# Kernel optimization log

Measured on AMD Instinct MI355X. Metric: run time of the kernel, lower is better.

## Reference

```python
import jax, jax.numpy as jnp
import numpy as np
from jax import lax

D = 96          # voxel grid side
N = 131072      # active voxels
C = 128         # channels
EPS = 1e-4
SLOPE_INNER = 0.05      # nn.LeakyReLU(0.05)
SLOPE_OUT = 1.0 / 3.0   # scn.LeakyReLU() default leakiness


def _build_nbr():
    rng = np.random.default_rng(0)
    lin = rng.choice(D ** 3, size=N, replace=False)
    coords = np.stack(np.unravel_index(lin, (D, D, D)), axis=1)  # [N,3]
    lut = -np.ones(D ** 3, dtype=np.int64)
    lut[lin] = np.arange(N)
    nbr = np.full((N, 27), -1, dtype=np.int64)
    k = 0
    for dx in (-1, 0, 1):
        for dy in (-1, 0, 1):
            for dz in (-1, 0, 1):
                nc = coords + np.array([dx, dy, dz])
                valid = ((nc >= 0) & (nc < D)).all(axis=1)
                li = nc[valid, 0] * D * D + nc[valid, 1] * D + nc[valid, 2]
                nbr[valid, k] = lut[li]
                k += 1
    return nbr


def setup_inputs() -> dict:
    key = jax.random.key(0)
    ks = jax.random.split(key, 4)
    ws = 1.0 / np.sqrt(27 * C)
    return {
        "features": jax.random.normal(ks[0], (N, C), jnp.float32),
        "nbr_idx": jnp.asarray(_build_nbr()),
        "w1": jax.random.normal(ks[1], (27, C, C), jnp.float32) * ws,
        "w2": jax.random.normal(ks[2], (27, C, C), jnp.float32) * ws,
        "w3": jax.random.normal(ks[3], (27, C, C), jnp.float32) * ws,
        "g1": jnp.ones((C,), jnp.float32), "b1": jnp.zeros((C,), jnp.float32),
        "g2": jnp.ones((C,), jnp.float32), "b2": jnp.zeros((C,), jnp.float32),
        "g3": jnp.ones((C,), jnp.float32), "b3": jnp.zeros((C,), jnp.float32),
    }


def _subm_conv(feat, nbr, W):
    # feat [N,Cin], nbr [N,27] (-1 = no active neighbor), W [27,Cin,Cout]
    mask = nbr >= 0
    safe = jnp.where(mask, nbr, 0)
    acc0 = jnp.zeros((feat.shape[0], W.shape[-1]), feat.dtype)

    def step(acc, inp):
        idx, m, Wk = inp  # idx [N], m [N], Wk [Cin,Cout]
        g = feat[idx] * m[:, None].astype(feat.dtype)  # gather + mask
        return acc + g @ Wk, None

    out, _ = lax.scan(step, acc0, (safe.T, mask.T, W))
    return out


def _bn(x, g, b):
    # BatchNorm1d with batch stats (track_running_stats=False), biased var
    mu = x.mean(axis=0)
    var = x.var(axis=0)
    return (x - mu) * lax.rsqrt(var + EPS) * g + b


def _lrelu(x, slope):
    return jnp.where(x >= 0, x, slope * x)


def reference(features, nbr_idx, w1, w2, w3, g1, b1, g2, b2, g3, b3):
    x = _lrelu(_bn(_subm_conv(features, nbr_idx, w1), g1, b1), SLOPE_INNER)
    res = x
    x = _lrelu(_bn(_subm_conv(x, nbr_idx, w2), g2, b2), SLOPE_INNER)
    x = _bn(_subm_conv(x, nbr_idx, w3), g3, b3)
    return _lrelu(x + res, SLOPE_OUT)
```

## Files before the change

### kernel.cpp

```cpp
#include <hip/hip_runtime.h>
#include <hip/hip_bf16.h>
#include <stdint.h>

#define NVOX 131072
#define CCH  128
#define EPSV 1e-4f

typedef __bf16 bf16_t;
typedef bf16_t bf16x8 __attribute__((ext_vector_type(8)));
typedef bf16_t bf16x4 __attribute__((ext_vector_type(4)));
typedef float  f32x4  __attribute__((ext_vector_type(4)));

__device__ __forceinline__ void async16(void* lds, const void* g) {
    __builtin_amdgcn_global_load_lds(
        (const __attribute__((address_space(1))) uint32_t*)g,
        (__attribute__((address_space(3))) uint32_t*)lds, 16, 0, 0);
}

__global__ void k_prep_feat(const float* __restrict__ f, bf16_t* __restrict__ fb) {
    int i = blockIdx.x * 256 + threadIdx.x;
    const float4* f4 = (const float4*)f;
    float4 v = f4[i];
    bf16x4 o;
    o[0] = (bf16_t)v.x; o[1] = (bf16_t)v.y; o[2] = (bf16_t)v.z; o[3] = (bf16_t)v.w;
    ((bf16x4*)fb)[i] = o;
}

__global__ void k_prep_misc(bf16_t* featb, bf16_t* xb1, bf16_t* xb2, float* stats) {
    int t = threadIdx.x;
    if (t < 128) {
        featb[(size_t)NVOX * CCH + t] = (bf16_t)0.0f;
        xb1[(size_t)NVOX * CCH + t]   = (bf16_t)0.0f;
        xb2[(size_t)NVOX * CCH + t]   = (bf16_t)0.0f;
    }
    for (int i = t; i < 768; i += 256) stats[i] = 0.0f;
}

__global__ void k_prep_w(const float* __restrict__ w0, const float* __restrict__ w1,
                         const float* __restrict__ w2, bf16_t* __restrict__ wbt) {
    int blk = blockIdx.x;
    int layer = blk / 27, k = blk % 27;
    const float* w = (layer == 0 ? w0 : (layer == 1 ? w1 : w2)) + k * 16384;
    __shared__ bf16_t tile[128][132];
    for (int e = threadIdx.x; e < 16384; e += 256) {
        int ci = e >> 7, co = e & 127;
        tile[co][ci] = (bf16_t)w[e];
    }
    __syncthreads();
    bf16_t* out = wbt + (size_t)blk * 16384;
    for (int e = threadIdx.x; e < 16384; e += 256) {
        int co = e >> 7, ci = e & 127;
        out[e] = tile[co][ci];
    }
}

__global__ __launch_bounds__(256, 3) void k_conv(
        const bf16_t* __restrict__ featb,
        const bf16_t* __restrict__ wbt,
        const int* __restrict__ nbr,
        float* __restrict__ out,
        float* __restrict__ stat)
{
    __shared__ uint32_t offs[27 * 128];
    __shared__ bf16_t smA[128 * 32];
    __shared__ bf16_t smB[128 * 32];
    __shared__ float ssum[128], ssq[128];

    const int tid = threadIdx.x;
    const int m0 = blockIdx.x << 7;

    if (tid < 128) { ssum[tid] = 0.0f; ssq[tid] = 0.0f; }

    for (int e = tid; e < 27 * 128; e += 256) {
        int row = e / 27, k = e - row * 27;
        int idx = nbr[(size_t)(m0 + row) * 27 + k];
        offs[(k << 7) + row] = ((uint32_t)(idx < 0 ? NVOX : idx)) << 8;
    }
    __syncthreads();

    const int l = tid & 63, w = tid >> 6;
    const int wm = w >> 1, wn = w & 1;
    const int lrow = l & 15, lq = l >> 4;

    const int srow = (w << 4) + (l >> 2);
    const int ssub = (l & 3) << 4;

    char* dstA0 = (char*)smA + (w << 10);
    char* dstA1 = (char*)smA + 4096 + (w << 10);
    char* dstB0 = (char*)smB + (w << 10);
    char* dstB1 = (char*)smB + 4096 + (w << 10);

    const char* fbase = (const char*)featb;
    const char* wbase = (const char*)wbt;

    f32x4 acc[4][4] = {};

    for (int k = 0; k < 27; ++k) {
        uint32_t offA0 = offs[(k << 7) + srow];
        uint32_t offA1 = offs[(k << 7) + srow + 64];
        const char* wk = wbase + ((size_t)k << 15);
        #pragma unroll
        for (int c = 0; c < 4; ++c) {
            const int cb = c << 6;
            __syncthreads();
            async16(dstA0, fbase + offA0 + cb + ssub);
            async16(dstA1, fbase + offA1 + cb + ssub);
            async16(dstB0, wk + (srow << 8) + cb + ssub);
            async16(dstB1, wk + ((srow + 64) << 8) + cb + ssub);
            __syncthreads();

            bf16x8 af[4], bfr[4];
            #pragma unroll
            for (int i = 0; i < 4; ++i) {
                af[i]  = *(const bf16x8*)((const char*)smA +
                          ((((wm << 6) + (i << 4) + lrow)) << 6) + (lq << 4));
                bfr[i] = *(const bf16x8*)((const char*)smB +
                          ((((wn << 6) + (i << 4) + lrow)) << 6) + (lq << 4));
            }
            #pragma unroll
            for (int i = 0; i < 4; ++i)
                #pragma unroll
                for (int j = 0; j < 4; ++j)
                    acc[i][j] = __builtin_amdgcn_mfma_f32_16x16x32_bf16(
                        af[i], bfr[j], acc[i][j], 0, 0, 0);
        }
    }

    float csum[4] = {0, 0, 0, 0}, csq[4] = {0, 0, 0, 0};
    #pragma unroll
    for (int j = 0; j < 4; ++j) {
        int col = (wn << 6) + (j << 4) + lrow;
        #pragma unroll
        for (int i = 0; i < 4; ++i) {
            int grow = m0 + (wm << 6) + (i << 4) + (lq << 2);
            #pragma unroll
            for (int r = 0; r < 4; ++r) {
                float v = acc[i][j][r];
                out[(size_t)(grow + r) * CCH + col] = v;
                csum[j] += v;
                csq[j]  += v * v;
            }
        }
    }
    #pragma unroll
    for (int j = 0; j < 4; ++j) {
        csum[j] += __shfl_xor(csum[j], 16, 64);
        csum[j] += __shfl_xor(csum[j], 32, 64);
        csq[j]  += __shfl_xor(csq[j], 16, 64);
        csq[j]  += __shfl_xor(csq[j], 32, 64);
    }
    if (lq == 0) {
        #pragma unroll
        for (int j = 0; j < 4; ++j) {
            int col = (wn << 6) + (j << 4) + lrow;
            atomicAdd(&ssum[col], csum[j]);
            atomicAdd(&ssq[col],  csq[j]);
        }
    }
    __syncthreads();
    if (tid < 128) {
        atomicAdd(&stat[tid],       ssum[tid]);
        atomicAdd(&stat[128 + tid], ssq[tid]);
    }
}

__global__ void k_bnact(const float* __restrict__ x, const float* __restrict__ stat,
                        const float* __restrict__ g, const float* __restrict__ b,
                        bf16_t* __restrict__ out, float slope) {
    __shared__ float sc[128], sh[128];
    int tid = threadIdx.x;
    if (tid < 128) {
        float mu  = stat[tid] * (1.0f / NVOX);
        float var = stat[128 + tid] * (1.0f / NVOX) - mu * mu;
        float inv = rsqrtf(var + EPSV);
        float s = g[tid] * inv;
        sc[tid] = s;
        sh[tid] = b[tid] - mu * s;
    }
    __syncthreads();
    int i = blockIdx.x * 256 + tid;
    float4 v = ((const float4*)x)[i];
    int c = (i << 2) & 127;
    float y0 = v.x * sc[c]     + sh[c];
    float y1 = v.y * sc[c + 1] + sh[c + 1];
    float y2 = v.z * sc[c + 2] + sh[c + 2];
    float y3 = v.w * sc[c + 3] + sh[c + 3];
    y0 = y0 >= 0.0f ? y0 : slope * y0;
    y1 = y1 >= 0.0f ? y1 : slope * y1;
    y2 = y2 >= 0.0f ? y2 : slope * y2;
    y3 = y3 >= 0.0f ? y3 : slope * y3;
    bf16x4 o;
    o[0] = (bf16_t)y0; o[1] = (bf16_t)y1; o[2] = (bf16_t)y2; o[3] = (bf16_t)y3;
    ((bf16x4*)out)[i] = o;
}

__global__ void k_final(const float* __restrict__ x, const float* __restrict__ stat,
                        const float* __restrict__ g, const float* __restrict__ b,
                        const bf16_t* __restrict__ res, float* __restrict__ out) {
    __shared__ float sc[128], sh[128];
    int tid = threadIdx.x;
    if (tid < 128) {
        float mu  = stat[tid] * (1.0f / NVOX);
        float var = stat[128 + tid] * (1.0f / NVOX) - mu * mu;
        float inv = rsqrtf(var + EPSV);
        float s = g[tid] * inv;
        sc[tid] = s;
        sh[tid] = b[tid] - mu * s;
    }
    __syncthreads();
    int i = blockIdx.x * 256 + tid;
    float4 v = ((const float4*)x)[i];
    bf16x4 r = ((const bf16x4*)res)[i];
    int c = (i << 2) & 127;
    float y0 = v.x * sc[c]     + sh[c]     + (float)r[0];
    float y1 = v.y * sc[c + 1] + sh[c + 1] + (float)r[1];
    float y2 = v.z * sc[c + 2] + sh[c + 2] + (float)r[2];
    float y3 = v.w * sc[c + 3] + sh[c + 3] + (float)r[3];
    const float k3 = 1.0f / 3.0f;
    y0 = y0 >= 0.0f ? y0 : k3 * y0;
    y1 = y1 >= 0.0f ? y1 : k3 * y1;
    y2 = y2 >= 0.0f ? y2 : k3 * y2;
    y3 = y3 >= 0.0f ? y3 : k3 * y3;
    float4 o; o.x = y0; o.y = y1; o.z = y2; o.w = y3;
    ((float4*)out)[i] = o;
}

extern "C" void kernel_launch(void* const* d_in, const int* in_sizes, int n_in,
                              void* d_out, int out_size, void* d_ws, size_t ws_size,
                              hipStream_t stream) {
    (void)in_sizes; (void)n_in; (void)out_size; (void)ws_size;
    const float* features = (const float*)d_in[0];
    const int*   nbr      = (const int*)d_in[1];
    const float* w1 = (const float*)d_in[2];
    const float* w2 = (const float*)d_in[3];
    const float* w3 = (const float*)d_in[4];
    const float* g1 = (const float*)d_in[5];
    const float* b1 = (const float*)d_in[6];
    const float* g2 = (const float*)d_in[7];
    const float* b2 = (const float*)d_in[8];
    const float* g3 = (const float*)d_in[9];
    const float* b3 = (const float*)d_in[10];

    char* ws = (char*)d_ws;
    const size_t SZ_FB = (size_t)(NVOX + 1) * CCH * 2;
    bf16_t* featb    = (bf16_t*)(ws);
    bf16_t* xb1      = (bf16_t*)(ws + SZ_FB);
    bf16_t* xb2      = (bf16_t*)(ws + 2 * SZ_FB);
    float*  conv_out = (float*)(ws + 3 * SZ_FB);
    bf16_t* wbt      = (bf16_t*)(ws + 3 * SZ_FB + (size_t)NVOX * CCH * 4);
    float*  stats    = (float*)(ws + 3 * SZ_FB + (size_t)NVOX * CCH * 4
                                + (size_t)3 * 27 * 128 * 128 * 2);

    k_prep_feat<<<16384, 256, 0, stream>>>(features, featb);
    k_prep_misc<<<1, 256, 0, stream>>>(featb, xb1, xb2, stats);
    k_prep_w<<<81, 256, 0, stream>>>(w1, w2, w3, wbt);

    k_conv<<<1024, 256, 0, stream>>>(featb, wbt, nbr, conv_out, stats);
    k_bnact<<<16384, 256, 0, stream>>>(conv_out, stats, g1, b1, xb1, 0.05f);

    k_conv<<<1024, 256, 0, stream>>>(xb1, wbt + (size_t)27 * 16384, nbr, conv_out, stats + 256);
    k_bnact<<<16384, 256, 0, stream>>>(conv_out, stats + 256, g2, b2, xb2, 0.05f);

    k_conv<<<1024, 256, 0, stream>>>(xb2, wbt + (size_t)2 * 27 * 16384, nbr, conv_out, stats + 512);
    k_final<<<16384, 256, 0, stream>>>(conv_out, stats + 512, g3, b3, xb1, (float*)d_out);
}
```

Measured before the change: 538.7 us.

## Triple-buffer conv LDS staging with async prefetch and XOR-swizzled layout

Replaces the single-buffer load/sync/compute loop in the sparse conv GEMM with a flattened 108-step pipeline that keeps two stages of gather and weight loads in flight across three LDS buffers. Only one barrier per step remains, gated by explicit vmcnt waits. It also XOR-swizzles the LDS layout to reduce bank conflicts on fragment reads and raises wave priority around the MFMA block. The extra LDS use forces launch bounds down from 3 to 2 blocks per CU, which lowers occupancy.

```diff
diff --git a/kernel.cpp b/kernel.cpp
--- a/kernel.cpp
+++ b/kernel.cpp
@@ -54,7 +54,7 @@
     }
 }
 
-__global__ __launch_bounds__(256, 3) void k_conv(
+__global__ __launch_bounds__(256, 2) void k_conv(
         const bf16_t* __restrict__ featb,
         const bf16_t* __restrict__ wbt,
         const int* __restrict__ nbr,
@@ -62,8 +62,8 @@
         float* __restrict__ stat)
 {
     __shared__ uint32_t offs[27 * 128];
-    __shared__ bf16_t smA[128 * 32];
-    __shared__ bf16_t smB[128 * 32];
+    __shared__ bf16_t smA[3][4096];
+    __shared__ bf16_t smB[3][4096];
     __shared__ float ssum[128], ssq[128];
 
     const int tid = threadIdx.x;
@@ -76,54 +76,84 @@
         int idx = nbr[(size_t)(m0 + row) * 27 + k];
         offs[(k << 7) + row] = ((uint32_t)(idx < 0 ? NVOX : idx)) << 8;
     }
-    __syncthreads();
 
     const int l = tid & 63, w = tid >> 6;
     const int wm = w >> 1, wn = w & 1;
     const int lrow = l & 15, lq = l >> 4;
 
     const int srow = (w << 4) + (l >> 2);
-    const int ssub = (l & 3) << 4;
-
-    char* dstA0 = (char*)smA + (w << 10);
-    char* dstA1 = (char*)smA + 4096 + (w << 10);
-    char* dstB0 = (char*)smB + (w << 10);
-    char* dstB1 = (char*)smB + 4096 + (w << 10);
+    const int ssub = (((l & 3) ^ ((l >> 3) & 3)) << 4);
+    const int cxor = (lq << 4) ^ ((((l & 15) >> 1) & 3) << 4);
 
     const char* fbase = (const char*)featb;
     const char* wbase = (const char*)wbt;
 
     f32x4 acc[4][4] = {};
 
-    for (int k = 0; k < 27; ++k) {
-        uint32_t offA0 = offs[(k << 7) + srow];
-        uint32_t offA1 = offs[(k << 7) + srow + 64];
+    auto ISSUE = [&](uint32_t a0, uint32_t a1, int k, int c, int b) {
+        const int cb = c << 6;
         const char* wk = wbase + ((size_t)k << 15);
-        #pragma unroll
-        for (int c = 0; c < 4; ++c) {
-            const int cb = c << 6;
-            __syncthreads();
-            async16(dstA0, fbase + offA0 + cb + ssub);
-            async16(dstA1, fbase + offA1 + cb + ssub);
-            async16(dstB0, wk + (srow << 8) + cb + ssub);
-            async16(dstB1, wk + ((srow + 64) << 8) + cb + ssub);
-            __syncthreads();
-
-            bf16x8 af[4], bfr[4];
+        char* dA = (char*)&smA[b][0] + (w << 10);
+        char* dB = (char*)&smB[b][0] + (w << 10);
+        async16(dA,        fbase + a0 + cb + ssub);
+        async16(dA + 4096, fbase + a1 + cb + ssub);
+        async16(dB,        wk + (srow << 8) + cb + ssub);
+        async16(dB + 4096, wk + ((srow + 64) << 8) + cb + ssub);
+    };
+
+    __syncthreads();
+
+    {
+        uint32_t a0 = offs[srow], a1 = offs[srow + 64];
+        ISSUE(a0, a1, 0, 0, 0);
+        ISSUE(a0, a1, 0, 1, 1);
+        asm volatile("s_waitcnt vmcnt(4)" ::: "memory");
+        __builtin_amdgcn_sched_barrier(0);
+        __builtin_amdgcn_s_barrier();
+    }
+
+    int cur = 0, nxt = 2;
+    for (int t = 0; t < 108; ++t) {
+        const bool do_stage = (t < 106);
+        uint32_t a0 = 0, a1 = 0; int k2 = 0, c2 = 0;
+        if (do_stage) {
+            const int t2 = t + 2;
+            k2 = t2 >> 2; c2 = t2 & 3;
+            a0 = offs[(k2 << 7) + srow];
+            a1 = offs[(k2 << 7) + srow + 64];
+        }
+
+        const char* bA = (const char*)&smA[cur][0];
+        const char* bB = (const char*)&smB[cur][0];
+        bf16x8 af[4], bfr[4];
+        #pragma unroll
+        for (int i = 0; i < 4; ++i) {
+            af[i]  = *(const bf16x8*)(bA + ((((wm << 6) + (i << 4) + lrow)) << 6) + cxor);
+            bfr[i] = *(const bf16x8*)(bB + ((((wn << 6) + (i << 4) + lrow)) << 6) + cxor);
+        }
+
+        if (do_stage) ISSUE(a0, a1, k2, c2, nxt);
+
+        __builtin_amdgcn_s_setprio(1);
+        #pragma unroll
+        for (int i = 0; i < 4; ++i)
             #pragma unroll
-            for (int i = 0; i < 4; ++i) {
-                af[i]  = *(const bf16x8*)((const char*)smA +
-                          ((((wm << 6) + (i << 4) + lrow)) << 6) + (lq << 4));
-                bfr[i] = *(const bf16x8*)((const char*)smB +
-                          ((((wn << 6) + (i << 4) + lrow)) << 6) + (lq << 4));
-            }
-            #pragma unroll
-            for (int i = 0; i < 4; ++i)
-                #pragma unroll
-                for (int j = 0; j < 4; ++j)
-                    acc[i][j] = __builtin_amdgcn_mfma_f32_16x16x32_bf16(
-                        af[i], bfr[j], acc[i][j], 0, 0, 0);
-        }
+            for (int j = 0; j < 4; ++j)
+                acc[i][j] = __builtin_amdgcn_mfma_f32_16x16x32_bf16(
+                    af[i], bfr[j], acc[i][j], 0, 0, 0);
+        __builtin_amdgcn_s_setprio(0);
+
+        if (t < 106) {
+            asm volatile("s_waitcnt vmcnt(4) lgkmcnt(0)" ::: "memory");
+            __builtin_amdgcn_sched_barrier(0);
+            __builtin_amdgcn_s_barrier();
+        } else if (t == 106) {
+            asm volatile("s_waitcnt vmcnt(0) lgkmcnt(0)" ::: "memory");
+            __builtin_amdgcn_sched_barrier(0);
+            __builtin_amdgcn_s_barrier();
+        }
+        cur = (cur == 2) ? 0 : cur + 1;
+        nxt = (nxt == 2) ? 0 : nxt + 1;
     }
 
     float csum[4] = {0, 0, 0, 0}, csq[4] = {0, 0, 0, 0};
```

After: 580.4 us. 7.7% more time.

## Software-pipeline sparse conv GEMM with multi-buffered async LDS loads and 512-thread tiles

Applied to the files above, without the earlier changes.

Rewrites the conv main loop so the async global-to-LDS gathers for upcoming K-chunks (triple-buffered A, double-buffered B) are issued while MFMAs run on the current chunk. This removes the two full barriers per chunk that previously serialized load and compute. Tiles grow to 256 rows with 512 threads, so each weight chunk is reused across twice as many rows. It also adds an XOR swizzle to cut LDS bank conflicts, reads neighbor indices straight from global instead of staging an offset table, and uses s_setprio around the MFMA bursts. The cost is larger LDS use per block, more complex hand-placed waitcnt and barrier logic, and fewer blocks in the grid.

```diff
diff --git a/kernel.cpp b/kernel.cpp
--- a/kernel.cpp
+++ b/kernel.cpp
@@ -54,77 +54,120 @@
     }
 }
 
-__global__ __launch_bounds__(256, 3) void k_conv(
+__global__ __launch_bounds__(512, 2) void k_conv(
         const bf16_t* __restrict__ featb,
         const bf16_t* __restrict__ wbt,
         const int* __restrict__ nbr,
         float* __restrict__ out,
         float* __restrict__ stat)
 {
-    __shared__ uint32_t offs[27 * 128];
-    __shared__ bf16_t smA[128 * 32];
-    __shared__ bf16_t smB[128 * 32];
-    __shared__ float ssum[128], ssq[128];
+    __shared__ __align__(16) char smem[65536];
+    char* smA = smem;
+    char* smB = smem + 49152;
 
     const int tid = threadIdx.x;
-    const int m0 = blockIdx.x << 7;
-
-    if (tid < 128) { ssum[tid] = 0.0f; ssq[tid] = 0.0f; }
-
-    for (int e = tid; e < 27 * 128; e += 256) {
-        int row = e / 27, k = e - row * 27;
-        int idx = nbr[(size_t)(m0 + row) * 27 + k];
-        offs[(k << 7) + row] = ((uint32_t)(idx < 0 ? NVOX : idx)) << 8;
-    }
-    __syncthreads();
+    const int m0 = blockIdx.x << 8;
 
     const int l = tid & 63, w = tid >> 6;
     const int wm = w >> 1, wn = w & 1;
     const int lrow = l & 15, lq = l >> 4;
 
-    const int srow = (w << 4) + (l >> 2);
-    const int ssub = (l & 3) << 4;
-
-    char* dstA0 = (char*)smA + (w << 10);
-    char* dstA1 = (char*)smA + 4096 + (w << 10);
-    char* dstB0 = (char*)smB + (w << 10);
-    char* dstB1 = (char*)smB + 4096 + (w << 10);
+    const int rA = tid >> 2;
+    const int swz  = (((tid & 3) ^ ((rA >> 1) & 3)) << 4);
+    const int cxor = ((lq ^ ((lrow >> 1) & 3)) << 4);
 
     const char* fbase = (const char*)featb;
     const char* wbase = (const char*)wbt;
+    const int* nb0 = nbr + (size_t)(m0 + rA) * 27;
+    const int* nb1 = nbr + (size_t)(m0 + rA + 128) * 27;
 
     f32x4 acc[4][4] = {};
 
-    for (int k = 0; k < 27; ++k) {
-        uint32_t offA0 = offs[(k << 7) + srow];
-        uint32_t offA1 = offs[(k << 7) + srow + 64];
-        const char* wk = wbase + ((size_t)k << 15);
+    auto B_ISSUE = [&](int bw, int kb, int cb) {
+        const char* wk = wbase + ((size_t)kb << 15);
+        char* dB = smB + (bw << 13) + (w << 10);
+        async16(dB, wk + (rA << 8) + (cb << 6) + swz);
+    };
+    auto A_ISSUE = [&](int aw, int ca, int ia0, int ia1) {
+        uint32_t o0 = ((uint32_t)(ia0 < 0 ? NVOX : ia0)) << 8;
+        uint32_t o1 = ((uint32_t)(ia1 < 0 ? NVOX : ia1)) << 8;
+        const int cb = ca << 6;
+        char* dA = smA + (aw << 14) + (w << 10);
+        async16(dA,        fbase + o0 + cb + swz);
+        async16(dA + 8192, fbase + o1 + cb + swz);
+    };
+
+    auto PHASE = [&](int a_rd, int b_rd,
+                     bool doB, int bw, int kb, int cb,
+                     bool doA, int aw, int ca, int ia0, int ia1,
+                     int wsel) {
+        const char* bA = smA + (a_rd << 14);
+        const char* bB = smB + (b_rd << 13);
+        bf16x8 af[4], bfr[4];
         #pragma unroll
-        for (int c = 0; c < 4; ++c) {
-            const int cb = c << 6;
-            __syncthreads();
-            async16(dstA0, fbase + offA0 + cb + ssub);
-            async16(dstA1, fbase + offA1 + cb + ssub);
-            async16(dstB0, wk + (srow << 8) + cb + ssub);
-            async16(dstB1, wk + ((srow + 64) << 8) + cb + ssub);
-            __syncthreads();
-
-            bf16x8 af[4], bfr[4];
+        for (int i = 0; i < 4; ++i) {
+            af[i]  = *(const bf16x8*)(bA + (((wm << 6) + (i << 4) + lrow) << 6) + cxor);
+            bfr[i] = *(const bf16x8*)(bB + (((wn << 6) + (i << 4) + lrow) << 6) + cxor);
+        }
+        if (doB) B_ISSUE(bw, kb, cb);
+        if (doA) A_ISSUE(aw, ca, ia0, ia1);
+        __builtin_amdgcn_sched_barrier(0);
+        __builtin_amdgcn_s_barrier();
+        asm volatile("s_waitcnt lgkmcnt(0)" ::: "memory");
+        __builtin_amdgcn_sched_barrier(0);
+        __builtin_amdgcn_s_setprio(1);
+        #pragma unroll
+        for (int i = 0; i < 4; ++i)
             #pragma unroll
-            for (int i = 0; i < 4; ++i) {
-                af[i]  = *(const bf16x8*)((const char*)smA +
-                          ((((wm << 6) + (i << 4) + lrow)) << 6) + (lq << 4));
-                bfr[i] = *(const bf16x8*)((const char*)smB +
-                          ((((wn << 6) + (i << 4) + lrow)) << 6) + (lq << 4));
-            }
-            #pragma unroll
-            for (int i = 0; i < 4; ++i)
-                #pragma unroll
-                for (int j = 0; j < 4; ++j)
-                    acc[i][j] = __builtin_amdgcn_mfma_f32_16x16x32_bf16(
-                        af[i], bfr[j], acc[i][j], 0, 0, 0);
+            for (int j = 0; j < 4; ++j)
+                acc[i][j] = __builtin_amdgcn_mfma_f32_16x16x32_bf16(
+                    af[i], bfr[j], acc[i][j], 0, 0, 0);
+        __builtin_amdgcn_s_setprio(0);
+        if (wsel == 0) {
+            asm volatile("s_waitcnt vmcnt(2)" ::: "memory");
+            __builtin_amdgcn_sched_barrier(0);
+            __builtin_amdgcn_s_barrier();
+        } else if (wsel == 1) {
+            asm volatile("s_waitcnt vmcnt(0)" ::: "memory");
+            __builtin_amdgcn_sched_barrier(0);
+            __builtin_amdgcn_s_barrier();
         }
-    }
+    };
+
+    int iA0 = nb0[0], iA1 = nb1[0];
+    int iB0 = nb0[1], iB1 = nb1[1];
+    __builtin_amdgcn_sched_barrier(0);
+    B_ISSUE(0, 0, 0);
+    A_ISSUE(0, 0, iA0, iA1);
+    A_ISSUE(1, 1, iA0, iA1);
+    asm volatile("s_waitcnt vmcnt(2)" ::: "memory");
+    __builtin_amdgcn_sched_barrier(0);
+    __builtin_amdgcn_s_barrier();
+
+    #pragma unroll 1
+    for (int u = 0; u < 26; ++u) {
+        const int ab  = u % 3;
+        const int ab1 = (ab == 2) ? 0 : ab + 1;
+        const int ab2 = (ab1 == 2) ? 0 : ab1 + 1;
+        const int kc = (u + 2 < 27) ? u + 2 : 26;
+        int iC0 = nb0[kc], iC1 = nb1[kc];
+        __builtin_amdgcn_sched_barrier(0);
+        PHASE(ab,  0, true, 1, u,     1, true, ab2, 2, iA0, iA1, 0);
+        PHASE(ab1, 1, true, 0, u,     2, true, ab,  3, iA0, iA1, 0);
+        PHASE(ab2, 0, true, 1, u,     3, true, ab1, 0, iB0, iB1, 0);
+        PHASE(ab,  1, true, 0, u + 1, 0, true, ab2, 1, iB0, iB1, 0);
+        iA0 = iB0; iA1 = iB1; iB0 = iC0; iB1 = iC1;
+    }
+    PHASE(2, 0, true,  1, 26, 1, true,  1, 2, iA0, iA1, 0);
+    PHASE(0, 1, true,  0, 26, 2, true,  2, 3, iA0, iA1, 0);
+    PHASE(1, 0, true,  1, 26, 3, false, 0, 0, 0, 0, 1);
+    PHASE(2, 1, false, 0, 0,  0, false, 0, 0, 0, 0, 2);
+
+    __syncthreads();
+    float* ssum = (float*)smA;
+    float* ssq  = ssum + 128;
+    if (tid < 128) { ssum[tid] = 0.0f; ssq[tid] = 0.0f; }
+    __syncthreads();
 
     float csum[4] = {0, 0, 0, 0}, csq[4] = {0, 0, 0, 0};
     #pragma unroll
@@ -255,12 +298,12 @@
     k_prep_misc<<<1, 256, 0, stream>>>(featb, xb1, xb2, stats);
     k_prep_w<<<81, 256, 0, stream>>>(w1, w2, w3, wbt);
 
-    k_conv<<<1024, 256, 0, stream>>>(featb, wbt, nbr, conv_out, stats);
+    k_conv<<<512, 512, 0, stream>>>(featb, wbt, nbr, conv_out, stats);
     k_bnact<<<16384, 256, 0, stream>>>(conv_out, stats, g1, b1, xb1, 0.05f);
 
-    k_conv<<<1024, 256, 0, stream>>>(xb1, wbt + (size_t)27 * 16384, nbr, conv_out, stats + 256);
+    k_conv<<<512, 512, 0, stream>>>(xb1, wbt + (size_t)27 * 16384, nbr, conv_out, stats + 256);
     k_bnact<<<16384, 256, 0, stream>>>(conv_out, stats + 256, g2, b2, xb2, 0.05f);
 
-    k_conv<<<1024, 256, 0, stream>>>(xb2, wbt + (size_t)2 * 27 * 16384, nbr, conv_out, stats + 512);
+    k_conv<<<512, 512, 0, stream>>>(xb2, wbt + (size_t)2 * 27 * 16384, nbr, conv_out, stats + 512);
     k_final<<<16384, 256, 0, stream>>>(conv_out, stats + 512, g3, b3, xb1, (float*)d_out);
 }
```

New measurement: 588.3 us. +9.2%, slower.

## Double-buffer conv LDS tiles with async prefetch, swizzle LDS, fold misc prep

Applied to the files above, without the earlier changes.

The conv kernel now double-buffers the A and B tiles in LDS. It issues async global-to-LDS loads for the next chunk before running the MFMAs on the current one, so the kernel needs one barrier per chunk instead of two. It drops the per-block offset table and reads neighbor indices directly with a one-step lookahead. It also XOR-swizzles the LDS layout to cut bank conflicts, raises the occupancy hint to 4 blocks per CU, and uses setprio around the MFMAs. The misc zero-init kernel is folded into an extra block of the weight-prep kernel to save one launch.

```diff
diff --git a/kernel.cpp b/kernel.cpp
--- a/kernel.cpp
+++ b/kernel.cpp
@@ -26,19 +26,20 @@
     ((bf16x4*)fb)[i] = o;
 }
 
-__global__ void k_prep_misc(bf16_t* featb, bf16_t* xb1, bf16_t* xb2, float* stats) {
-    int t = threadIdx.x;
-    if (t < 128) {
-        featb[(size_t)NVOX * CCH + t] = (bf16_t)0.0f;
-        xb1[(size_t)NVOX * CCH + t]   = (bf16_t)0.0f;
-        xb2[(size_t)NVOX * CCH + t]   = (bf16_t)0.0f;
-    }
-    for (int i = t; i < 768; i += 256) stats[i] = 0.0f;
-}
-
 __global__ void k_prep_w(const float* __restrict__ w0, const float* __restrict__ w1,
-                         const float* __restrict__ w2, bf16_t* __restrict__ wbt) {
+                         const float* __restrict__ w2, bf16_t* __restrict__ wbt,
+                         bf16_t* featb, bf16_t* xb1, bf16_t* xb2, float* stats) {
     int blk = blockIdx.x;
+    if (blk == 81) {
+        int t = threadIdx.x;
+        if (t < 128) {
+            featb[(size_t)NVOX * CCH + t] = (bf16_t)0.0f;
+            xb1[(size_t)NVOX * CCH + t]   = (bf16_t)0.0f;
+            xb2[(size_t)NVOX * CCH + t]   = (bf16_t)0.0f;
+        }
+        for (int i = t; i < 768; i += 256) stats[i] = 0.0f;
+        return;
+    }
     int layer = blk / 27, k = blk % 27;
     const float* w = (layer == 0 ? w0 : (layer == 1 ? w1 : w2)) + k * 16384;
     __shared__ bf16_t tile[128][132];
@@ -54,76 +55,94 @@
     }
 }
 
-__global__ __launch_bounds__(256, 3) void k_conv(
+__global__ __launch_bounds__(256, 4) void k_conv(
         const bf16_t* __restrict__ featb,
         const bf16_t* __restrict__ wbt,
         const int* __restrict__ nbr,
         float* __restrict__ out,
         float* __restrict__ stat)
 {
-    __shared__ uint32_t offs[27 * 128];
-    __shared__ bf16_t smA[128 * 32];
-    __shared__ bf16_t smB[128 * 32];
-    __shared__ float ssum[128], ssq[128];
+    __shared__ __align__(16) char smem[33792];
+    float* ssum = (float*)(smem + 32768);
+    float* ssq  = ssum + 128;
 
     const int tid = threadIdx.x;
     const int m0 = blockIdx.x << 7;
 
     if (tid < 128) { ssum[tid] = 0.0f; ssq[tid] = 0.0f; }
-
-    for (int e = tid; e < 27 * 128; e += 256) {
-        int row = e / 27, k = e - row * 27;
-        int idx = nbr[(size_t)(m0 + row) * 27 + k];
-        offs[(k << 7) + row] = ((uint32_t)(idx < 0 ? NVOX : idx)) << 8;
-    }
-    __syncthreads();
 
     const int l = tid & 63, w = tid >> 6;
     const int wm = w >> 1, wn = w & 1;
     const int lrow = l & 15, lq = l >> 4;
 
     const int srow = (w << 4) + (l >> 2);
-    const int ssub = (l & 3) << 4;
-
-    char* dstA0 = (char*)smA + (w << 10);
-    char* dstA1 = (char*)smA + 4096 + (w << 10);
-    char* dstB0 = (char*)smB + (w << 10);
-    char* dstB1 = (char*)smB + 4096 + (w << 10);
+    const int ssub = (((l & 3) ^ ((l >> 3) & 3)) << 4);
+    const int cxor = ((lq ^ ((lrow >> 1) & 3)) << 4);
 
     const char* fbase = (const char*)featb;
     const char* wbase = (const char*)wbt;
+    const int* nb0 = nbr + (size_t)(m0 + srow) * 27;
+    const int* nb1 = nbr + (size_t)(m0 + srow + 64) * 27;
 
     f32x4 acc[4][4] = {};
 
+    auto ISSUE = [&](int b, int kk, int cc, int i0, int i1) {
+        uint32_t o0 = ((uint32_t)(i0 < 0 ? NVOX : i0)) << 8;
+        uint32_t o1 = ((uint32_t)(i1 < 0 ? NVOX : i1)) << 8;
+        const int cb = cc << 6;
+        const char* wk = wbase + ((size_t)kk << 15);
+        char* dA = smem + (b << 13) + (w << 10);
+        char* dB = smem + 16384 + (b << 13) + (w << 10);
+        async16(dA,        fbase + o0 + cb + ssub);
+        async16(dA + 4096, fbase + o1 + cb + ssub);
+        async16(dB,        wk + (srow << 8) + cb + ssub);
+        async16(dB + 4096, wk + ((srow + 64) << 8) + cb + ssub);
+    };
+
+    int iA0 = nb0[0], iA1 = nb1[0];
+    __builtin_amdgcn_sched_barrier(0);
+    ISSUE(0, 0, 0, iA0, iA1);
+    asm volatile("s_waitcnt vmcnt(0)" ::: "memory");
+    __builtin_amdgcn_sched_barrier(0);
+    __builtin_amdgcn_s_barrier();
+
+    #pragma unroll 1
     for (int k = 0; k < 27; ++k) {
-        uint32_t offA0 = offs[(k << 7) + srow];
-        uint32_t offA1 = offs[(k << 7) + srow + 64];
-        const char* wk = wbase + ((size_t)k << 15);
+        int iN0 = iA0, iN1 = iA1;
+        if (k < 26) { iN0 = nb0[k + 1]; iN1 = nb1[k + 1]; }
         #pragma unroll
         for (int c = 0; c < 4; ++c) {
-            const int cb = c << 6;
-            __syncthreads();
-            async16(dstA0, fbase + offA0 + cb + ssub);
-            async16(dstA1, fbase + offA1 + cb + ssub);
-            async16(dstB0, wk + (srow << 8) + cb + ssub);
-            async16(dstB1, wk + ((srow + 64) << 8) + cb + ssub);
-            __syncthreads();
-
+            const int cur = c & 1;
+            const bool last = (k == 26) && (c == 3);
+            const char* bA = smem + (cur << 13);
+            const char* bB = smem + 16384 + (cur << 13);
             bf16x8 af[4], bfr[4];
             #pragma unroll
             for (int i = 0; i < 4; ++i) {
-                af[i]  = *(const bf16x8*)((const char*)smA +
-                          ((((wm << 6) + (i << 4) + lrow)) << 6) + (lq << 4));
-                bfr[i] = *(const bf16x8*)((const char*)smB +
-                          ((((wn << 6) + (i << 4) + lrow)) << 6) + (lq << 4));
-            }
+                af[i]  = *(const bf16x8*)(bA + (((wm << 6) + (i << 4) + lrow) << 6) + cxor);
+                bfr[i] = *(const bf16x8*)(bB + (((wn << 6) + (i << 4) + lrow) << 6) + cxor);
+            }
+            if (!last) {
+                if (c == 3) ISSUE(cur ^ 1, k + 1, 0, iN0, iN1);
+                else        ISSUE(cur ^ 1, k, c + 1, iA0, iA1);
+            }
+            asm volatile("s_waitcnt lgkmcnt(0)" ::: "memory");
+            __builtin_amdgcn_sched_barrier(0);
+            __builtin_amdgcn_s_setprio(1);
             #pragma unroll
             for (int i = 0; i < 4; ++i)
                 #pragma unroll
                 for (int j = 0; j < 4; ++j)
                     acc[i][j] = __builtin_amdgcn_mfma_f32_16x16x32_bf16(
                         af[i], bfr[j], acc[i][j], 0, 0, 0);
-        }
+            __builtin_amdgcn_s_setprio(0);
+            if (!last) {
+                asm volatile("s_waitcnt vmcnt(0)" ::: "memory");
+                __builtin_amdgcn_sched_barrier(0);
+                __builtin_amdgcn_s_barrier();
+            }
+        }
+        iA0 = iN0; iA1 = iN1;
     }
 
     float csum[4] = {0, 0, 0, 0}, csq[4] = {0, 0, 0, 0};
@@ -252,8 +271,7 @@
                                 + (size_t)3 * 27 * 128 * 128 * 2);
 
     k_prep_feat<<<16384, 256, 0, stream>>>(features, featb);
-    k_prep_misc<<<1, 256, 0, stream>>>(featb, xb1, xb2, stats);
-    k_prep_w<<<81, 256, 0, stream>>>(w1, w2, w3, wbt);
+    k_prep_w<<<82, 256, 0, stream>>>(w1, w2, w3, wbt, featb, xb1, xb2, stats);
 
     k_conv<<<1024, 256, 0, stream>>>(featb, wbt, nbr, conv_out, stats);
     k_bnact<<<16384, 256, 0, stream>>>(conv_out, stats, g1, b1, xb1, 0.05f);
```

New measurement: 1.010 ms. 1.87x slower.
